# Performance work log

Hardware: AMD Instinct MI355X
Metric: run time of the kernel (lower is better)

Reference implementation:

```python
import jax, jax.numpy as jnp
import numpy as np


def hadamard(D):
    # Sylvester Hadamard: H[i,j] = (-1)^popcount(i & j), normalized by sqrt(D)
    x = np.arange(D)[:, None] & np.arange(D)[None, :]
    par = np.zeros_like(x)
    for _ in range(int(np.log2(D)) + 1):
        par ^= x & 1
        x >>= 1
    return ((1.0 - 2.0 * par) / np.sqrt(D)).astype(np.float32)


def setup_inputs() -> dict:
    key = jax.random.key(0)
    ks = jax.random.split(key, 6)
    K, M, D, T = 4, 32, 2048, 128
    z = jax.random.normal(ks[0], (K, M, D, T), dtype=jnp.float32)
    d1 = jax.random.normal(ks[1], (D, 1), dtype=jnp.float32)
    d2 = jax.random.normal(ks[2], (D, 1), dtype=jnp.float32)
    d3 = jax.random.normal(ks[3], (D, 1), dtype=jnp.float32)
    b = jax.random.normal(ks[4], (D, 1), dtype=jnp.float32)
    sldj = jax.random.normal(ks[5], (K * M,), dtype=jnp.float32)
    return {"z": z, "d1": d1, "d2": d2, "d3": d3, "b": b,
            "sum_log_det_jacobians": sldj}


def reference(z, d1, d2, d3, b, sum_log_det_jacobians):
    K, M, D, T = z.shape
    H = jnp.asarray(hadamard(D), dtype=z.dtype)
    # A = H @ D3 @ H @ D2 @ H @ D1
    #   H @ diag(d)  == H * d.T (scale columns)
    #   diag(d) @ X  == d * X   (scale rows)
    A = H @ (d3 * (H @ (d2 * (H * d1[:, 0][None, :]))))
    # apply: tensordot(A, z, [[1],[2]]) then transpose to (K,M,D,T), add bias
    z_out = jnp.einsum('de,kmet->kmdt', A, z) + b[None, None, :, :]
    # log|det A| = sum_i log|d1_i| + log|d2_i| + log|d3_i|  (H is orthogonal)
    log_det_A = (jnp.sum(jnp.log(jnp.abs(d1)))
                 + jnp.sum(jnp.log(jnp.abs(d2)))
                 + jnp.sum(jnp.log(jnp.abs(d3))))
    sldj = sum_log_det_jacobians + log_det_A * jnp.ones((K * M,), dtype=z.dtype)
    return z_out, sldj
```

## Files before the change

kernel.cpp:

```cpp
#include <hip/hip_runtime.h>
#include <math.h>

#define D_DIM 2048
#define T_DIM 128
#define TT 16

typedef __attribute__((address_space(1))) const unsigned int gu32;
typedef __attribute__((address_space(3))) unsigned int su32;

__device__ __forceinline__ int sw1(int x) { return x ^ ((x >> 5) & 1); }
__device__ __forceinline__ int sw2(int x) { return x ^ ((x >> 4) & 1); }

#define BFLY(MM)                                              \
    _Pragma("unroll")                                         \
    for (int i_ = 0; i_ < 64; ++i_) {                         \
        if ((i_ & (MM)) == 0) {                               \
            float a_ = v[i_], b_ = v[i_ | (MM)];              \
            v[i_] = a_ + b_;                                  \
            v[i_ | (MM)] = a_ - b_;                           \
        }                                                     \
    }

__device__ __forceinline__ void barx() {
    asm volatile("s_waitcnt lgkmcnt(0)" ::: "memory");
    __builtin_amdgcn_s_barrier();
    asm volatile("" ::: "memory");
}
#define VWAIT(N) asm volatile("s_waitcnt vmcnt(" #N ")" ::: "memory")

__global__ __launch_bounds__(512, 2)
void fwht_apply_kernel(const float* __restrict__ z,
                       const float* __restrict__ d1,
                       const float* __restrict__ d2,
                       const float* __restrict__ d3,
                       const float* __restrict__ bvec,
                       const float* __restrict__ sldj_in,
                       float* __restrict__ out) {
    extern __shared__ float sh[];
    float* buf0 = sh;
    float* buf1 = sh + 16384;
    float* d1l  = sh + 32768;
    float* d2l  = sh + 34816;
    float* d3l  = sh + 36864;
    float* bl   = sh + 38912;
    const int tid = threadIdx.x;

    if (blockIdx.x == 256) {
        float acc = 0.0f;
        for (int i = tid; i < D_DIM; i += 512)
            acc += logf(fabsf(d1[i])) + logf(fabsf(d2[i])) + logf(fabsf(d3[i]));
        sh[tid] = acc;
        __syncthreads();
        #pragma unroll
        for (int sft = 256; sft > 0; sft >>= 1) {
            if (tid < sft) sh[tid] += sh[tid + sft];
            __syncthreads();
        }
        if (tid < 128)
            out[(size_t)4 * 32 * 2048 * 128 + tid] = sldj_in[tid] + sh[0];
        return;
    }

    const int r    = tid >> 4;
    const int tt   = tid & 15;
    const int b    = blockIdx.x;
    const int wid  = tid >> 6;
    const int lane = tid & 63;
    const int q    = lane >> 2;
    const int c    = lane & 3;
    const float s  = 0.022097086912079608f;

    for (int k = tid; k < D_DIM; k += 512) {
        d1l[k] = d1[k] * s;
        d2l[k] = d2[k] * s;
        d3l[k] = d3[k] * s;
        bl[k]  = bvec[k];
    }

    auto issue = [&](float* buf, int tau, int h) {
        const float* zs = z + ((size_t)(tau >> 3) << 18) + ((tau & 7) << 4) + (c << 2);
        #pragma unroll
        for (int i = 0; i < 8; ++i) {
            const int n = (wid << 3) | i;
            const int e = (n << 5) | (h << 4) | q;
            __builtin_amdgcn_global_load_lds((gu32*)(zs + (size_t)e * T_DIM),
                                             (su32*)(buf + (n << 8)), 16, 0, 0);
        }
    };

    issue(buf0, b << 2, 0);

    #pragma unroll 1
    for (int ti = 0; ti < 4; ++ti) {
        const int tau = (b << 2) | ti;
        float v[64];

        barx();
        issue(buf1, tau, 1);
        VWAIT(8);
        barx();
        if (r < 16) {
            #pragma unroll
            for (int j = 0; j < 64; ++j)
                v[j] = buf0[(((j << 4) | (r & 15)) << 4) + tt] * d1l[(j << 5) | r];
        }
        barx();
        if (ti < 3) { issue(buf0, tau + 1, 0); VWAIT(8); }
        else        { VWAIT(0); }
        barx();
        if (r >= 16) {
            #pragma unroll
            for (int j = 0; j < 64; ++j)
                v[j] = buf1[(((j << 4) | (r & 15)) << 4) + tt] * d1l[(j << 5) | r];
        }
        barx();

        float* tl = buf1;

        BFLY(1) BFLY(2) BFLY(4) BFLY(8) BFLY(16) BFLY(32)

        #pragma unroll
        for (int j = 0; j < 32; ++j)
            tl[sw1((j << 5) | r) * TT + tt] = v[j];
        barx();
        #pragma unroll
        for (int j = 0; j < 32; ++j)
            v[j] = tl[sw1(j | (r << 5)) * TT + tt];
        barx();
        #pragma unroll
        for (int j = 32; j < 64; ++j)
            tl[sw1(((j & 31) << 5) | r) * TT + tt] = v[j];
        barx();
        #pragma unroll
        for (int j = 32; j < 64; ++j)
            v[j] = tl[sw1((j & 31) | (r << 5)) * TT + tt];
        barx();

        BFLY(1) BFLY(2) BFLY(4) BFLY(8) BFLY(16)
        {
            const float4* q0 = (const float4*)(d2l + (r << 5));
            const float4* q1 = (const float4*)(d2l + 1024 + (r << 5));
            #pragma unroll
            for (int qq = 0; qq < 8; ++qq) {
                float4 a = q0[qq];
                v[4*qq+0] *= a.x; v[4*qq+1] *= a.y;
                v[4*qq+2] *= a.z; v[4*qq+3] *= a.w;
                float4 cc = q1[qq];
                v[32+4*qq+0] *= cc.x; v[32+4*qq+1] *= cc.y;
                v[32+4*qq+2] *= cc.z; v[32+4*qq+3] *= cc.w;
            }
        }
        BFLY(1) BFLY(2) BFLY(4) BFLY(8) BFLY(16) BFLY(32)

        #pragma unroll
        for (int j = 0; j < 64; j += 2)
            tl[sw2(((j >> 1) & 15) | (r << 4) | ((j >> 5) << 9)) * TT + tt] = v[j];
        barx();
        #pragma unroll
        for (int j = 0; j < 64; j += 2)
            v[j] = tl[sw2((((j >> 1) & 31) << 4) | (r & 15) | ((r >> 4) << 9)) * TT + tt];
        barx();
        #pragma unroll
        for (int j = 1; j < 64; j += 2)
            tl[sw2(((j >> 1) & 15) | (r << 4) | ((j >> 5) << 9)) * TT + tt] = v[j];
        barx();
        #pragma unroll
        for (int j = 1; j < 64; j += 2)
            v[j] = tl[sw2((((j >> 1) & 31) << 4) | (r & 15) | ((r >> 4) << 9)) * TT + tt];
        barx();

        BFLY(2) BFLY(4) BFLY(8) BFLY(16) BFLY(32)
        {
            const int eRest = ((r & 15) << 1) | ((r >> 4) << 10);
            #pragma unroll
            for (int m = 0; m < 32; ++m) {
                float2 a = *(const float2*)(d3l + ((m << 5) | eRest));
                v[2*m]   *= a.x;
                v[2*m+1] *= a.y;
            }
        }
        BFLY(2) BFLY(4) BFLY(8) BFLY(16) BFLY(32) BFLY(1)

        #pragma unroll
        for (int j = 0; j < 64; j += 2)
            tl[sw2((((j >> 1) & 31) << 4) | (r & 15) | ((r >> 4) << 9)) * TT + tt] = v[j];
        barx();
        #pragma unroll
        for (int j = 0; j < 64; j += 2)
            v[j] = tl[sw2(((j >> 1) & 15) | (r << 4) | ((j >> 5) << 9)) * TT + tt];
        barx();
        #pragma unroll
        for (int j = 1; j < 64; j += 2)
            tl[sw2((((j >> 1) & 31) << 4) | (r & 15) | ((r >> 4) << 9)) * TT + tt] = v[j];
        barx();
        #pragma unroll
        for (int j = 1; j < 64; j += 2)
            v[j] = tl[sw2(((j >> 1) & 15) | (r << 4) | ((j >> 5) << 9)) * TT + tt];

        BFLY(2) BFLY(4) BFLY(8) BFLY(16) BFLY(32)

        float* ob = out + ((size_t)(tau >> 3) << 18) + ((tau & 7) << 4) + tt;
        {
            const float4* q0 = (const float4*)(bl + (r << 5));
            const float4* q1 = (const float4*)(bl + 1024 + (r << 5));
            #pragma unroll
            for (int qq = 0; qq < 8; ++qq) {
                float4 a = q0[qq];
                const int e0 = (r << 5) + 4*qq;
                ob[(size_t)(e0+0) * T_DIM] = v[4*qq+0] + a.x;
                ob[(size_t)(e0+1) * T_DIM] = v[4*qq+1] + a.y;
                ob[(size_t)(e0+2) * T_DIM] = v[4*qq+2] + a.z;
                ob[(size_t)(e0+3) * T_DIM] = v[4*qq+3] + a.w;
                float4 cc = q1[qq];
                const int e1 = 1024 + (r << 5) + 4*qq;
                ob[(size_t)(e1+0) * T_DIM] = v[32+4*qq+0] + cc.x;
                ob[(size_t)(e1+1) * T_DIM] = v[32+4*qq+1] + cc.y;
                ob[(size_t)(e1+2) * T_DIM] = v[32+4*qq+2] + cc.z;
                ob[(size_t)(e1+3) * T_DIM] = v[32+4*qq+3] + cc.w;
            }
        }
    }
}

extern "C" void kernel_launch(void* const* d_in, const int* in_sizes, int n_in,
                              void* d_out, int out_size, void* d_ws, size_t ws_size,
                              hipStream_t stream) {
    const float* z    = (const float*)d_in[0];
    const float* d1   = (const float*)d_in[1];
    const float* d2   = (const float*)d_in[2];
    const float* d3   = (const float*)d_in[3];
    const float* bvec = (const float*)d_in[4];
    const float* sldj = (const float*)d_in[5];
    float* out = (float*)d_out;

    hipFuncSetAttribute((const void*)fwht_apply_kernel,
                        hipFuncAttributeMaxDynamicSharedMemorySize, 163840);

    fwht_apply_kernel<<<257, 512, 163840, stream>>>(z, d1, d2, d3, bvec, sldj, out);
}
```

Before: 314.7 us.

## Restructure LDS layout to load full tile and prefetch next tile mid-pipeline

Changes the z staging so both halves of a 2048x16 tile are loaded into one contiguous LDS region up front. All 512 threads now read their 64 values in one pass. The first and second transposes are collapsed from two half-passes into single full passes with new XOR swizzles, which cuts the number of barriers. Prefetch of the next tile's two halves is moved into the middle of the compute, after each region of LDS becomes free, so loads overlap the later butterflies. The hipFuncSetAttribute call is also cached so it runs once. The risks are extra bank conflicts under the new swizzles and tighter LDS reuse ordering.

Result: slower. 648.3 us (+106.0%).

```diff
diff --git a/kernel.cpp b/kernel.cpp
--- a/kernel.cpp
+++ b/kernel.cpp
@@ -8,7 +8,8 @@
 typedef __attribute__((address_space(1))) const unsigned int gu32;
 typedef __attribute__((address_space(3))) unsigned int su32;
 
-__device__ __forceinline__ int sw1(int x) { return x ^ ((x >> 5) & 1); }
+__device__ __forceinline__ int rw1(int e) { return e ^ ((e >> 5) & 1); }
+__device__ __forceinline__ int rw2(int e) { return e ^ ((e >> 5) & 1) ^ ((e >> 1) & 1); }
 __device__ __forceinline__ int sw2(int x) { return x ^ ((x >> 4) & 1); }
 
 #define BFLY(MM)                                              \
@@ -37,12 +38,10 @@
                        const float* __restrict__ sldj_in,
                        float* __restrict__ out) {
     extern __shared__ float sh[];
-    float* buf0 = sh;
-    float* buf1 = sh + 16384;
-    float* d1l  = sh + 32768;
-    float* d2l  = sh + 34816;
-    float* d3l  = sh + 36864;
-    float* bl   = sh + 38912;
+    float* d1l = sh + 32768;
+    float* d2l = sh + 34816;
+    float* d3l = sh + 36864;
+    float* bl  = sh + 38912;
     const int tid = threadIdx.x;
 
     if (blockIdx.x == 256) {
@@ -77,63 +76,47 @@
         bl[k]  = bvec[k];
     }
 
-    auto issue = [&](float* buf, int tau, int h) {
+    auto issue = [&](int tau, int h) {
         const float* zs = z + ((size_t)(tau >> 3) << 18) + ((tau & 7) << 4) + (c << 2);
+        float* buf = sh + (h << 14);
         #pragma unroll
         for (int i = 0; i < 8; ++i) {
             const int n = (wid << 3) | i;
-            const int e = (n << 5) | (h << 4) | q;
+            const int e = (h << 10) | (n << 4) | q;
             __builtin_amdgcn_global_load_lds((gu32*)(zs + (size_t)e * T_DIM),
                                              (su32*)(buf + (n << 8)), 16, 0, 0);
         }
     };
 
-    issue(buf0, b << 2, 0);
+    issue(b << 2, 0);
+    issue(b << 2, 1);
+    VWAIT(0);
+    barx();
 
     #pragma unroll 1
     for (int ti = 0; ti < 4; ++ti) {
         const int tau = (b << 2) | ti;
+        const int eR  = ((r & 15) << 1) | ((r >> 4) << 10);
         float v[64];
 
-        barx();
-        issue(buf1, tau, 1);
-        VWAIT(8);
-        barx();
-        if (r < 16) {
-            #pragma unroll
-            for (int j = 0; j < 64; ++j)
-                v[j] = buf0[(((j << 4) | (r & 15)) << 4) + tt] * d1l[(j << 5) | r];
-        }
-        barx();
-        if (ti < 3) { issue(buf0, tau + 1, 0); VWAIT(8); }
-        else        { VWAIT(0); }
-        barx();
-        if (r >= 16) {
-            #pragma unroll
-            for (int j = 0; j < 64; ++j)
-                v[j] = buf1[(((j << 4) | (r & 15)) << 4) + tt] * d1l[(j << 5) | r];
-        }
-        barx();
-
-        float* tl = buf1;
-
+        VWAIT(16);
+        barx();
+
+        #pragma unroll
+        for (int j = 0; j < 64; ++j) {
+            const int e = (j << 5) | r;
+            v[j] = sh[(e << 4) + tt] * d1l[e];
+        }
         BFLY(1) BFLY(2) BFLY(4) BFLY(8) BFLY(16) BFLY(32)
-
-        #pragma unroll
-        for (int j = 0; j < 32; ++j)
-            tl[sw1((j << 5) | r) * TT + tt] = v[j];
-        barx();
-        #pragma unroll
-        for (int j = 0; j < 32; ++j)
-            v[j] = tl[sw1(j | (r << 5)) * TT + tt];
-        barx();
-        #pragma unroll
-        for (int j = 32; j < 64; ++j)
-            tl[sw1(((j & 31) << 5) | r) * TT + tt] = v[j];
-        barx();
-        #pragma unroll
-        for (int j = 32; j < 64; ++j)
-            v[j] = tl[sw1((j & 31) | (r << 5)) * TT + tt];
+        barx();
+
+        #pragma unroll
+        for (int j = 0; j < 64; ++j)
+            sh[(rw1((j << 5) | r) << 4) + tt] = v[j];
+        barx();
+        #pragma unroll
+        for (int j = 0; j < 64; ++j)
+            v[j] = sh[(rw1((j & 31) | ((j >> 5) << 10) | (r << 5)) << 4) + tt];
         barx();
 
         BFLY(1) BFLY(2) BFLY(4) BFLY(8) BFLY(16)
@@ -153,28 +136,21 @@
         BFLY(1) BFLY(2) BFLY(4) BFLY(8) BFLY(16) BFLY(32)
 
         #pragma unroll
-        for (int j = 0; j < 64; j += 2)
-            tl[sw2(((j >> 1) & 15) | (r << 4) | ((j >> 5) << 9)) * TT + tt] = v[j];
-        barx();
-        #pragma unroll
-        for (int j = 0; j < 64; j += 2)
-            v[j] = tl[sw2((((j >> 1) & 31) << 4) | (r & 15) | ((r >> 4) << 9)) * TT + tt];
-        barx();
-        #pragma unroll
-        for (int j = 1; j < 64; j += 2)
-            tl[sw2(((j >> 1) & 15) | (r << 4) | ((j >> 5) << 9)) * TT + tt] = v[j];
-        barx();
-        #pragma unroll
-        for (int j = 1; j < 64; j += 2)
-            v[j] = tl[sw2((((j >> 1) & 31) << 4) | (r & 15) | ((r >> 4) << 9)) * TT + tt];
-        barx();
+        for (int j = 0; j < 64; ++j)
+            sh[(rw2((j & 31) | ((j >> 5) << 10) | (r << 5)) << 4) + tt] = v[j];
+        barx();
+        #pragma unroll
+        for (int j = 0; j < 64; ++j)
+            v[j] = sh[(rw2(((j >> 1) << 5) | (j & 1) | eR) << 4) + tt];
+        barx();
+
+        if (ti < 3) issue(tau + 1, 0);
 
         BFLY(2) BFLY(4) BFLY(8) BFLY(16) BFLY(32)
         {
-            const int eRest = ((r & 15) << 1) | ((r >> 4) << 10);
             #pragma unroll
             for (int m = 0; m < 32; ++m) {
-                float2 a = *(const float2*)(d3l + ((m << 5) | eRest));
+                float2 a = *(const float2*)(d3l + ((m << 5) | eR));
                 v[2*m]   *= a.x;
                 v[2*m+1] *= a.y;
             }
@@ -182,20 +158,18 @@
         BFLY(2) BFLY(4) BFLY(8) BFLY(16) BFLY(32) BFLY(1)
 
         #pragma unroll
-        for (int j = 0; j < 64; j += 2)
-            tl[sw2((((j >> 1) & 31) << 4) | (r & 15) | ((r >> 4) << 9)) * TT + tt] = v[j];
-        barx();
-        #pragma unroll
-        for (int j = 0; j < 64; j += 2)
-            v[j] = tl[sw2(((j >> 1) & 15) | (r << 4) | ((j >> 5) << 9)) * TT + tt];
-        barx();
-        #pragma unroll
-        for (int j = 1; j < 64; j += 2)
-            tl[sw2((((j >> 1) & 31) << 4) | (r & 15) | ((r >> 4) << 9)) * TT + tt] = v[j];
-        barx();
-        #pragma unroll
-        for (int j = 1; j < 64; j += 2)
-            v[j] = tl[sw2(((j >> 1) & 15) | (r << 4) | ((j >> 5) << 9)) * TT + tt];
+        for (int h2 = 0; h2 < 2; ++h2) {
+            #pragma unroll
+            for (int j = h2; j < 64; j += 2)
+                sh[((1024 + sw2(((j >> 1) << 4) | (r & 15) | ((r >> 4) << 9))) << 4) + tt] = v[j];
+            barx();
+            #pragma unroll
+            for (int j = h2; j < 64; j += 2)
+                v[j] = sh[((1024 + sw2(((j >> 1) & 15) | (r << 4) | ((j >> 5) << 9))) << 4) + tt];
+            barx();
+        }
+
+        if (ti < 3) issue(tau + 1, 1);
 
         BFLY(2) BFLY(4) BFLY(8) BFLY(16) BFLY(32)
 
@@ -233,8 +207,12 @@
     const float* sldj = (const float*)d_in[5];
     float* out = (float*)d_out;
 
-    hipFuncSetAttribute((const void*)fwht_apply_kernel,
-                        hipFuncAttributeMaxDynamicSharedMemorySize, 163840);
+    static bool attr_set = false;
+    if (!attr_set) {
+        hipFuncSetAttribute((const void*)fwht_apply_kernel,
+                            hipFuncAttributeMaxDynamicSharedMemorySize, 163840);
+        attr_set = true;
+    }
 
     fwht_apply_kernel<<<257, 512, 163840, stream>>>(z, d1, d2, d3, bvec, sldj, out);
 }
```
